# Performance work log

Hardware: AMD Instinct MI355X
Metric: run time of the kernel (lower is better)

The kernel has to match this reference:

```python
import jax, jax.numpy as jnp
import numpy as np

NE = 8192       # number of mesh elements
B = 64          # batch of density fields
AVG_DEG = 32    # neighbors per element within filter radius
NNZ = NE * AVG_DEG
NEG_SLOPE = 0.001


def setup_inputs() -> dict:
    key = jax.random.key(0)
    kx, kw, ks, ki = jax.random.split(key, 4)
    x = jax.random.normal(kx, (B, NE), dtype=jnp.float32)
    fc1_weight = jax.random.normal(kw, (NE, NE), dtype=jnp.float32) * (1.0 / np.sqrt(NE))
    # sparse weights initialized uniform(-bound, bound), bound = sqrt(2/Ne)
    bound = float(np.sqrt(2.0 / NE))
    sparse_weights = jax.random.uniform(ks, (NNZ,), dtype=jnp.float32,
                                        minval=-bound, maxval=bound)
    # static COO pattern (row, col) derived from mesh connectivity Rij < Rmin
    sparse_indices = jax.random.randint(ki, (2, NNZ), 0, NE, dtype=jnp.int64)
    return {"x": x, "fc1_weight": fc1_weight,
            "sparse_weights": sparse_weights, "sparse_indices": sparse_indices}


def reference(x, fc1_weight, sparse_weights, sparse_indices):
    # dense layer: h[b, i] = sum_k x[b, k] * W[i, k]
    h = x @ fc1_weight.T                         # [B, Ne]
    rows = sparse_indices[0]                     # [nnz]
    cols = sparse_indices[1]                     # [nnz]
    # sparse mm: out[b, j] = sum_{(i,j) in pattern} h[b, i] * w_{ij}
    contrib = h[:, rows] * sparse_weights        # [B, nnz] gather + scale
    out = jnp.zeros((x.shape[0], fc1_weight.shape[0]), dtype=h.dtype)
    out = out.at[:, cols].add(contrib)           # scatter-add over columns
    # leaky_relu, negative_slope = 0.001
    return jnp.where(out >= 0, out, NEG_SLOPE * out)
```

## Files before the change

### kernel.cpp

```cpp
#include <hip/hip_runtime.h>
#include <hip/hip_bf16.h>

#define NE 8192
#define BATCH 64
#define NNZT (NE * 32)
#define KSPLIT 4
#define KCH (NE / KSPLIT)
#define BK 128
#define NSTEP (KCH / BK)
#define TN 128

typedef float f32x2 __attribute__((ext_vector_type(2)));
typedef float f32x4 __attribute__((ext_vector_type(4)));
typedef short s16x8 __attribute__((ext_vector_type(8)));

__device__ __forceinline__ unsigned f2bf(float f) {
  unsigned u = __builtin_bit_cast(unsigned, f);
  return (u + 0x7FFFu + ((u >> 16) & 1u)) >> 16;
}

__global__ void k_convert_x(const float* __restrict__ x, unsigned short* __restrict__ xb) {
  int i = (blockIdx.x * 256 + threadIdx.x) * 4;
  float4 v = *reinterpret_cast<const float4*>(x + i);
  *reinterpret_cast<ushort4*>(xb + i) =
      make_ushort4((unsigned short)f2bf(v.x), (unsigned short)f2bf(v.y),
                   (unsigned short)f2bf(v.z), (unsigned short)f2bf(v.w));
}

__global__ void k_zero(float* __restrict__ p) {
  int i = (blockIdx.x * 256 + threadIdx.x) * 4;
  *reinterpret_cast<float4*>(p + i) = make_float4(0.f, 0.f, 0.f, 0.f);
}

__global__ __launch_bounds__(512, 2) void k_dense(const unsigned short* __restrict__ xb,
                                                  const float* __restrict__ W,
                                                  float* __restrict__ ht) {
  __shared__ __align__(16) char smem[98304];
  const int tid = threadIdx.x;
  const int wv = tid >> 6, l = tid & 63;
  const int kq = blockIdx.x & (KSPLIT - 1);
  const int i0 = (blockIdx.x >> 2) * TN;
  const int k0 = kq * KCH;

  const float* wsrc = W + (size_t)(i0 + wv * 16) * NE + k0 + l * 2;
  const unsigned short* xsrc = xb + (size_t)(wv * 8) * NE + k0 + l * 2;

  const int r16 = l & 15, q = l >> 4;
  const int fxor = (r16 & 7) << 4;
  const int wrow = wv * 16 + r16;

  f32x4 acc[4] = {};
  f32x2 wA[16], wB[16];
  unsigned xA[8], xB[8];

#define LOADW(WR, XR, s)                                                        \
  do {                                                                          \
    _Pragma("unroll") for (int j = 0; j < 16; ++j)                              \
        WR[j] = *reinterpret_cast<const f32x2*>(wsrc + (size_t)j * NE + (s)*BK); \
    _Pragma("unroll") for (int j = 0; j < 8; ++j)                               \
        XR[j] = *reinterpret_cast<const unsigned*>(xsrc + (size_t)j * NE + (s)*BK); \
    __builtin_amdgcn_sched_barrier(0);                                          \
  } while (0)

#define STORE(WR, XR, buf)                                                      \
  do {                                                                          \
    _Pragma("unroll") for (int j = 0; j < 16; ++j) {                            \
      const int r_ = wv * 16 + j;                                               \
      const int co_ = (l * 4) ^ ((r_ & 7) << 4);                                \
      unsigned pw_ = f2bf(WR[j][0]) | (f2bf(WR[j][1]) << 16);                   \
      *reinterpret_cast<unsigned*>(smem + (buf)*32768 + r_ * 256 + co_) = pw_;  \
    }                                                                           \
    _Pragma("unroll") for (int j = 0; j < 8; ++j) {                             \
      const int r_ = wv * 8 + j;                                                \
      const int co_ = (l * 4) ^ ((r_ & 7) << 4);                                \
      *reinterpret_cast<unsigned*>(smem + 65536 + (buf)*16384 + r_ * 256 + co_) = XR[j]; \
    }                                                                           \
    __builtin_amdgcn_sched_barrier(0);                                          \
  } while (0)

#define COMPUTE(buf)                                                            \
  do {                                                                          \
    _Pragma("unroll") for (int ks = 0; ks < 4; ++ks) {                          \
      const int col_ = (ks * 64 + q * 16) ^ fxor;                               \
      s16x8 bw_ = *reinterpret_cast<const s16x8*>(smem + (buf)*32768 + wrow * 256 + col_); \
      _Pragma("unroll") for (int g = 0; g < 4; ++g) {                           \
        s16x8 a_ = *reinterpret_cast<const s16x8*>(smem + 65536 + (buf)*16384 + \
                                                   (g * 16 + r16) * 256 + col_); \
        acc[g] = __builtin_amdgcn_mfma_f32_16x16x32_bf16(a_, bw_, acc[g], 0, 0, 0); \
      }                                                                         \
    }                                                                           \
    __builtin_amdgcn_sched_barrier(0);                                          \
  } while (0)

#define SBAR()                                              \
  do {                                                      \
    asm volatile("s_waitcnt lgkmcnt(0)" ::: "memory");      \
    __builtin_amdgcn_s_barrier();                           \
    __builtin_amdgcn_sched_barrier(0);                      \
  } while (0)

  LOADW(wA, xA, 0);
  LOADW(wB, xB, 1);
  STORE(wA, xA, 0);
  SBAR();

  for (int s = 0; s < NSTEP; s += 2) {
    if (s + 2 < NSTEP) LOADW(wA, xA, s + 2);
    if (s + 1 < NSTEP) STORE(wB, xB, 1);
    COMPUTE(0);
    SBAR();
    if (s + 3 < NSTEP) LOADW(wB, xB, s + 3);
    if (s + 2 < NSTEP) STORE(wA, xA, 0);
    COMPUTE(1);
    SBAR();
  }

#undef LOADW
#undef STORE
#undef COMPUTE
#undef SBAR

#pragma unroll
  for (int g = 0; g < 4; ++g) {
    float* hp = ht + (size_t)(i0 + wrow) * BATCH + g * 16 + q * 4;
#pragma unroll
    for (int j = 0; j < 4; ++j) atomicAdd(hp + j, acc[g][j]);
  }
}

__global__ void k_scatter(const float* __restrict__ ht, const float* __restrict__ sw,
                          const int* __restrict__ rows, const int* __restrict__ cols,
                          float* __restrict__ out_t) {
  const int w = (blockIdx.x * 256 + threadIdx.x) >> 6;
  const int lane = threadIdx.x & 63;
  const int n0 = w * (NNZT / 4096);
#pragma unroll 4
  for (int n = n0; n < n0 + (NNZT / 4096); ++n) {
    const int r = rows[n];
    const int c = cols[n];
    const float wv = sw[n];
    atomicAdd(out_t + (size_t)c * BATCH + lane, ht[(size_t)r * BATCH + lane] * wv);
  }
}

__global__ void k_final(const float* __restrict__ out_t, float* __restrict__ out) {
  __shared__ float tile[64][65];
  const int t = threadIdx.x;
  const int j0 = blockIdx.x * 64;
  {
    const int jl = t >> 2, b0 = (t & 3) * 16;
    const float* src = out_t + (size_t)(j0 + jl) * BATCH + b0;
#pragma unroll
    for (int e = 0; e < 16; e += 4) {
      float4 v = *reinterpret_cast<const float4*>(src + e);
      tile[jl][b0 + e + 0] = v.x;
      tile[jl][b0 + e + 1] = v.y;
      tile[jl][b0 + e + 2] = v.z;
      tile[jl][b0 + e + 3] = v.w;
    }
  }
  __syncthreads();
  {
    const int bl = t >> 2, js = (t & 3) * 16;
    float* dst = out + (size_t)bl * NE + j0 + js;
#pragma unroll
    for (int e = 0; e < 16; e += 4) {
      float a0 = tile[js + e + 0][bl];
      float a1 = tile[js + e + 1][bl];
      float a2 = tile[js + e + 2][bl];
      float a3 = tile[js + e + 3][bl];
      float4 v;
      v.x = a0 >= 0.f ? a0 : 0.001f * a0;
      v.y = a1 >= 0.f ? a1 : 0.001f * a1;
      v.z = a2 >= 0.f ? a2 : 0.001f * a2;
      v.w = a3 >= 0.f ? a3 : 0.001f * a3;
      *reinterpret_cast<float4*>(dst + e) = v;
    }
  }
}

extern "C" void kernel_launch(void* const* d_in, const int* in_sizes, int n_in,
                              void* d_out, int out_size, void* d_ws, size_t ws_size,
                              hipStream_t stream) {
  const float* x = (const float*)d_in[0];
  const float* W = (const float*)d_in[1];
  const float* sw = (const float*)d_in[2];
  const int* idx = (const int*)d_in[3];
  float* out = (float*)d_out;

  char* ws = (char*)d_ws;
  float* ht = (float*)ws;
  float* out_t = (float*)(ws + (2 << 20));
  unsigned short* xbf = (unsigned short*)(ws + (4 << 20));

  k_convert_x<<<512, 256, 0, stream>>>(x, xbf);
  k_zero<<<1024, 256, 0, stream>>>((float*)ws);
  k_dense<<<256, 512, 0, stream>>>(xbf, W, ht);
  k_scatter<<<1024, 256, 0, stream>>>(ht, sw, idx, idx + NNZT, out_t);
  k_final<<<128, 256, 0, stream>>>(out_t, out);
}
```

Measured before the change: 143.3 us.

## Keep x slice resident in LDS, stream W tiles with deeper K-split

Restructures the dense GEMM so each block loads its bf16 x K-slice into shared memory once and keeps it resident. Only W is streamed, in 64-wide K steps across four 64-row sub-tiles, with partial results flushed by atomics after each sub-tile. K-split goes from 4 to 16, which doubles the grid to 512 blocks, and launch bounds now target 4 blocks per CU to improve occupancy on the bandwidth-bound W stream. In exchange there are many more atomic adds into ht, and the W loads shrink to scalar per-lane floats.

```diff
diff --git a/kernel.cpp b/kernel.cpp
--- a/kernel.cpp
+++ b/kernel.cpp
@@ -4,14 +4,14 @@
 #define NE 8192
 #define BATCH 64
 #define NNZT (NE * 32)
-#define KSPLIT 4
+#define KSPLIT 16
 #define KCH (NE / KSPLIT)
-#define BK 128
-#define NSTEP (KCH / BK)
-#define TN 128
-
-typedef float f32x2 __attribute__((ext_vector_type(2)));
+#define BK 64
+#define SUBT 4
+#define MTOT (SUBT * (KCH / BK))
+
 typedef float f32x4 __attribute__((ext_vector_type(4)));
+typedef unsigned u32x4 __attribute__((ext_vector_type(4)));
 typedef short s16x8 __attribute__((ext_vector_type(8)));
 
 __device__ __forceinline__ unsigned f2bf(float f) {
@@ -32,64 +32,81 @@
   *reinterpret_cast<float4*>(p + i) = make_float4(0.f, 0.f, 0.f, 0.f);
 }
 
-__global__ __launch_bounds__(512, 2) void k_dense(const unsigned short* __restrict__ xb,
+__global__ __launch_bounds__(512, 4) void k_dense(const unsigned short* __restrict__ xb,
                                                   const float* __restrict__ W,
                                                   float* __restrict__ ht) {
-  __shared__ __align__(16) char smem[98304];
+  __shared__ __align__(16) char smem[81920];
   const int tid = threadIdx.x;
   const int wv = tid >> 6, l = tid & 63;
   const int kq = blockIdx.x & (KSPLIT - 1);
-  const int i0 = (blockIdx.x >> 2) * TN;
+  const int I0 = (blockIdx.x >> 4) * (SUBT * 64);
   const int k0 = kq * KCH;
-
-  const float* wsrc = W + (size_t)(i0 + wv * 16) * NE + k0 + l * 2;
-  const unsigned short* xsrc = xb + (size_t)(wv * 8) * NE + k0 + l * 2;
-
   const int r16 = l & 15, q = l >> 4;
   const int fxor = (r16 & 7) << 4;
-  const int wrow = wv * 16 + r16;
-
-  f32x4 acc[4] = {};
-  f32x2 wA[16], wB[16];
-  unsigned xA[8], xB[8];
-
-#define LOADW(WR, XR, s)                                                        \
-  do {                                                                          \
-    _Pragma("unroll") for (int j = 0; j < 16; ++j)                              \
-        WR[j] = *reinterpret_cast<const f32x2*>(wsrc + (size_t)j * NE + (s)*BK); \
+  const int wrow = (wv & 3) * 16 + r16;
+  const int bg = wv >> 2;
+  const int xrow0 = bg * 32 + r16;
+
+  {
+    u32x4 xr[8];
+#pragma unroll
+    for (int it = 0; it < 8; ++it) {
+      const int c = it * 512 + tid, row = c >> 6, cpos = c & 63;
+      xr[it] = *reinterpret_cast<const u32x4*>(xb + (size_t)row * NE + k0 + cpos * 8);
+    }
+#pragma unroll
+    for (int it = 0; it < 8; ++it) {
+      const int c = it * 512 + tid, row = c >> 6, cpos = c & 63;
+      *reinterpret_cast<u32x4*>(smem + row * 1024 + ((cpos * 16) ^ ((row & 7) << 4))) = xr[it];
+    }
+  }
+
+  const float* wbase = W + (size_t)(I0 + wv * 8) * NE + k0 + l;
+
+  float wAr[8], wBr[8];
+  f32x4 acc0 = {}, acc1 = {};
+
+#define LOADW(WR, m)                                                            \
+  do {                                                                          \
     _Pragma("unroll") for (int j = 0; j < 8; ++j)                               \
-        XR[j] = *reinterpret_cast<const unsigned*>(xsrc + (size_t)j * NE + (s)*BK); \
+        WR[j] = *(wbase + (size_t)(((m) >> 3) * 64 + j) * NE + ((m)&7) * 64);   \
     __builtin_amdgcn_sched_barrier(0);                                          \
   } while (0)
 
-#define STORE(WR, XR, buf)                                                      \
-  do {                                                                          \
-    _Pragma("unroll") for (int j = 0; j < 16; ++j) {                            \
-      const int r_ = wv * 16 + j;                                               \
-      const int co_ = (l * 4) ^ ((r_ & 7) << 4);                                \
-      unsigned pw_ = f2bf(WR[j][0]) | (f2bf(WR[j][1]) << 16);                   \
-      *reinterpret_cast<unsigned*>(smem + (buf)*32768 + r_ * 256 + co_) = pw_;  \
-    }                                                                           \
+#define STOREW(WR, buf)                                                         \
+  do {                                                                          \
     _Pragma("unroll") for (int j = 0; j < 8; ++j) {                             \
-      const int r_ = wv * 8 + j;                                                \
-      const int co_ = (l * 4) ^ ((r_ & 7) << 4);                                \
-      *reinterpret_cast<unsigned*>(smem + 65536 + (buf)*16384 + r_ * 256 + co_) = XR[j]; \
+      *reinterpret_cast<unsigned short*>(smem + 65536 + (buf)*8192 +            \
+                                         (wv * 8 + j) * 128 + ((l * 2) ^ (j << 4))) = \
+          (unsigned short)f2bf(WR[j]);                                          \
     }                                                                           \
     __builtin_amdgcn_sched_barrier(0);                                          \
   } while (0)
 
-#define COMPUTE(buf)                                                            \
-  do {                                                                          \
-    _Pragma("unroll") for (int ks = 0; ks < 4; ++ks) {                          \
-      const int col_ = (ks * 64 + q * 16) ^ fxor;                               \
-      s16x8 bw_ = *reinterpret_cast<const s16x8*>(smem + (buf)*32768 + wrow * 256 + col_); \
-      _Pragma("unroll") for (int g = 0; g < 4; ++g) {                           \
-        s16x8 a_ = *reinterpret_cast<const s16x8*>(smem + 65536 + (buf)*16384 + \
-                                                   (g * 16 + r16) * 256 + col_); \
-        acc[g] = __builtin_amdgcn_mfma_f32_16x16x32_bf16(a_, bw_, acc[g], 0, 0, 0); \
-      }                                                                         \
+#define COMPUTE(buf, m)                                                         \
+  do {                                                                          \
+    _Pragma("unroll") for (int ks = 0; ks < 2; ++ks) {                          \
+      const int cw_ = (ks * 64 + q * 16) ^ fxor;                                \
+      s16x8 bw_ = *reinterpret_cast<const s16x8*>(smem + 65536 + (buf)*8192 +   \
+                                                  wrow * 128 + cw_);            \
+      const int cx_ = (((m)&7) * 128 + ks * 64 + q * 16) ^ fxor;                \
+      s16x8 a0_ = *reinterpret_cast<const s16x8*>(smem + xrow0 * 1024 + cx_);   \
+      s16x8 a1_ = *reinterpret_cast<const s16x8*>(smem + (xrow0 + 16) * 1024 + cx_); \
+      acc0 = __builtin_amdgcn_mfma_f32_16x16x32_bf16(a0_, bw_, acc0, 0, 0, 0);  \
+      acc1 = __builtin_amdgcn_mfma_f32_16x16x32_bf16(a1_, bw_, acc1, 0, 0, 0);  \
     }                                                                           \
     __builtin_amdgcn_sched_barrier(0);                                          \
+  } while (0)
+
+#define DUMP(t)                                                                 \
+  do {                                                                          \
+    float* hp_ = ht + (size_t)(I0 + (t)*64 + wrow) * BATCH + bg * 32 + q * 4;   \
+    _Pragma("unroll") for (int j = 0; j < 4; ++j) {                             \
+      atomicAdd(hp_ + j, acc0[j]);                                              \
+      atomicAdd(hp_ + 16 + j, acc1[j]);                                         \
+    }                                                                           \
+    acc0 = (f32x4){};                                                           \
+    acc1 = (f32x4){};                                                           \
   } while (0)
 
 #define SBAR()                                              \
@@ -99,33 +116,28 @@
     __builtin_amdgcn_sched_barrier(0);                      \
   } while (0)
 
-  LOADW(wA, xA, 0);
-  LOADW(wB, xB, 1);
-  STORE(wA, xA, 0);
+  LOADW(wAr, 0);
+  LOADW(wBr, 1);
+  STOREW(wAr, 0);
   SBAR();
 
-  for (int s = 0; s < NSTEP; s += 2) {
-    if (s + 2 < NSTEP) LOADW(wA, xA, s + 2);
-    if (s + 1 < NSTEP) STORE(wB, xB, 1);
-    COMPUTE(0);
+  for (int m = 0; m < MTOT; m += 2) {
+    if (m + 2 < MTOT) LOADW(wAr, m + 2);
+    if (m + 1 < MTOT) STOREW(wBr, 1);
+    COMPUTE(0, m);
     SBAR();
-    if (s + 3 < NSTEP) LOADW(wB, xB, s + 3);
-    if (s + 2 < NSTEP) STORE(wA, xA, 0);
-    COMPUTE(1);
+    if (m + 3 < MTOT) LOADW(wBr, m + 3);
+    if (m + 2 < MTOT) STOREW(wAr, 0);
+    COMPUTE(1, m + 1);
+    if (((m + 1) & 7) == 7) DUMP((m + 1) >> 3);
     SBAR();
   }
 
 #undef LOADW
-#undef STORE
+#undef STOREW
 #undef COMPUTE
+#undef DUMP
 #undef SBAR
-
-#pragma unroll
-  for (int g = 0; g < 4; ++g) {
-    float* hp = ht + (size_t)(i0 + wrow) * BATCH + g * 16 + q * 4;
-#pragma unroll
-    for (int j = 0; j < 4; ++j) atomicAdd(hp + j, acc[g][j]);
-  }
 }
 
 __global__ void k_scatter(const float* __restrict__ ht, const float* __restrict__ sw,
@@ -195,7 +207,7 @@
 
   k_convert_x<<<512, 256, 0, stream>>>(x, xbf);
   k_zero<<<1024, 256, 0, stream>>>((float*)ws);
-  k_dense<<<256, 512, 0, stream>>>(xbf, W, ht);
+  k_dense<<<512, 512, 0, stream>>>(xbf, W, ht);
   k_scatter<<<1024, 256, 0, stream>>>(ht, sw, idx, idx + NNZT, out_t);
   k_final<<<128, 256, 0, stream>>>(out_t, out);
 }
```

After: 201.8 us. +40.8%, slower.
